# Kernel optimization log

Measured on AMD Instinct MI355X. Metric: run time of the kernel, lower is better.

Reference implementation:

```python
import jax, jax.numpy as jnp
import numpy as np

N = 500_000
B = 8192
D = 128
EPS = 1e-5


def setup_inputs() -> dict:
    key = jax.random.key(0)
    ks = jax.random.split(key, 8)
    h = jax.random.normal(ks[0], (N, D), dtype=jnp.float32)
    batch = jnp.sort(jax.random.randint(ks[1], (N,), 0, B)).astype(jnp.int64)
    vn_h = jax.random.normal(ks[2], (B, D), dtype=jnp.float32)
    # layer 0 MLP params: Linear(D,D) -> LayerNorm(D) -> ReLU -> Linear(D,D)
    W1 = jax.random.normal(ks[3], (D, D), dtype=jnp.float32) * 0.02
    b1 = jnp.zeros((D,), dtype=jnp.float32)
    ln_g = jnp.ones((D,), dtype=jnp.float32)
    ln_b = jnp.zeros((D,), dtype=jnp.float32)
    W2 = jax.random.normal(ks[4], (D, D), dtype=jnp.float32) * 0.02
    b2 = jnp.zeros((D,), dtype=jnp.float32)
    return {"h": h, "batch": batch, "vn_h": vn_h, "W1": W1, "b1": b1,
            "ln_g": ln_g, "ln_b": ln_b, "W2": W2, "b2": b2}


def _layernorm(x, g, b):
    mu = jnp.mean(x, axis=-1, keepdims=True)
    var = jnp.mean(jnp.square(x - mu), axis=-1, keepdims=True)
    return (x - mu) * jax.lax.rsqrt(var + EPS) * g + b


def reference(h, batch, vn_h, W1, b1, ln_g, ln_b, W2, b2):
    batch = batch.astype(jnp.int32)
    # global_mean_pool: segment mean of node features per graph  [B, D]
    seg_sum = jax.ops.segment_sum(h, batch, num_segments=B)
    counts = jax.ops.segment_sum(jnp.ones((h.shape[0],), h.dtype), batch, num_segments=B)
    pooled = seg_sum / jnp.maximum(counts, 1.0)[:, None]
    vn_h_new = pooled + vn_h
    # vn MLP: Linear -> LayerNorm -> ReLU -> Linear
    x = vn_h_new @ W1.T + b1
    x = jax.nn.relu(_layernorm(x, ln_g, ln_b))
    vn_out = x @ W2.T + b2                      # [B, D]
    h_out = h + vn_out[batch]                   # broadcast gather back to nodes
    return h_out, vn_out
```

## Files before the change

### kernel.cpp

```cpp
#include <hip/hip_runtime.h>

#define DIM 128
#define EPS 1e-5f

typedef short           bf16x8 __attribute__((ext_vector_type(8)));
typedef unsigned short  u16x8  __attribute__((ext_vector_type(8)));
typedef float           f32x4  __attribute__((ext_vector_type(4)));

__device__ __forceinline__ unsigned short f2b(float f) {
    unsigned int u = __builtin_bit_cast(unsigned int, f);
    unsigned int r = (u + 0x7FFFu + ((u >> 16) & 1u)) >> 16;
    return (unsigned short)r;
}
__device__ __forceinline__ bf16x8 ldw8(const float* __restrict__ p) {
    f32x4 a = *reinterpret_cast<const f32x4*>(p);
    f32x4 b = *reinterpret_cast<const f32x4*>(p + 4);
    bf16x8 r;
    #pragma unroll
    for (int j = 0; j < 4; ++j) {
        r[j]     = (short)f2b(a[j]);
        r[j + 4] = (short)f2b(b[j]);
    }
    return r;
}

__global__ __launch_bounds__(256) void k_fused(
    const float* __restrict__ h, const int* __restrict__ batch,
    const float* __restrict__ vn,
    const float* __restrict__ W1, const float* __restrict__ b1,
    const float* __restrict__ lng, const float* __restrict__ lnb,
    const float* __restrict__ W2, const float* __restrict__ b2v,
    float* __restrict__ vn_out, float* __restrict__ h_out, int n_nodes)
{
    __shared__ int sb[17];
    __shared__ unsigned short xtile[16][136];
    __shared__ float vtile[16][132];

    const int tid = threadIdx.x;
    const int G0  = blockIdx.x * 16;

    if (tid < 17) {
        const int target = G0 + tid;
        int lo = 0, hi = n_nodes;
        while (lo < hi) {
            int mid = (lo + hi) >> 1;
            if (batch[mid] < target) lo = mid + 1; else hi = mid;
        }
        sb[tid] = lo;
    }
    __syncthreads();

    const int gi = tid >> 4;
    const int j  = tid & 15;
    const int s = sb[gi], e = sb[gi + 1];

    f32x4 a0 = (f32x4){0.f, 0.f, 0.f, 0.f};
    f32x4 a1 = (f32x4){0.f, 0.f, 0.f, 0.f};
    for (int n = s; n < e; ++n) {
        const float* p = h + (size_t)n * DIM + j * 8;
        a0 += *reinterpret_cast<const f32x4*>(p);
        a1 += *reinterpret_cast<const f32x4*>(p + 4);
    }
    const int cnt = e - s;
    const float inv = 1.0f / (float)(cnt > 1 ? cnt : 1);
    const float* vp = vn + (size_t)(G0 + gi) * DIM + j * 8;
    f32x4 v0 = *reinterpret_cast<const f32x4*>(vp);
    f32x4 v1 = *reinterpret_cast<const f32x4*>(vp + 4);
    u16x8 xv;
    #pragma unroll
    for (int q = 0; q < 4; ++q) {
        xv[q]     = f2b(fmaf(a0[q], inv, v0[q]));
        xv[q + 4] = f2b(fmaf(a1[q], inv, v1[q]));
    }
    *reinterpret_cast<u16x8*>(&xtile[gi][j * 8]) = xv;
    __syncthreads();

    if (tid < 64) {
        const int lane  = tid;
        const int row16 = lane & 15;
        const int kgrp  = lane >> 4;

        bf16x8 afrag[4];
        #pragma unroll
        for (int kk = 0; kk < 4; ++kk)
            afrag[kk] = *reinterpret_cast<const bf16x8*>(&xtile[row16][kgrp * 8 + kk * 32]);

        f32x4 acc[8];
        #pragma unroll
        for (int t = 0; t < 8; ++t) acc[t] = (f32x4){0.f, 0.f, 0.f, 0.f};
        #pragma unroll
        for (int t = 0; t < 8; ++t) {
            const float* wp = W1 + (size_t)(t * 16 + row16) * DIM + kgrp * 8;
            #pragma unroll
            for (int kk = 0; kk < 4; ++kk) {
                bf16x8 bfrag = ldw8(wp + kk * 32);
                acc[t] = __builtin_amdgcn_mfma_f32_16x16x32_bf16(afrag[kk], bfrag, acc[t], 0, 0, 0);
            }
        }

        float b1f[8], gf[8], bf_[8], b2f8[8];
        #pragma unroll
        for (int t = 0; t < 8; ++t) {
            const int f = t * 16 + row16;
            b1f[t]  = b1[f];
            gf[t]   = lng[f];
            bf_[t]  = lnb[f];
            b2f8[t] = b2v[f];
        }
        #pragma unroll
        for (int t = 0; t < 8; ++t)
            #pragma unroll
            for (int r = 0; r < 4; ++r) acc[t][r] += b1f[t];

        #pragma unroll
        for (int r = 0; r < 4; ++r) {
            float sm = 0.f, ss = 0.f;
            #pragma unroll
            for (int t = 0; t < 8; ++t) { sm += acc[t][r]; ss += acc[t][r] * acc[t][r]; }
            #pragma unroll
            for (int m = 1; m <= 8; m <<= 1) {
                sm += __shfl_xor(sm, m);
                ss += __shfl_xor(ss, m);
            }
            const float mu  = sm * (1.0f / 128.0f);
            const float var = ss * (1.0f / 128.0f) - mu * mu;
            const float rs  = rsqrtf(var + EPS);
            const int   gm  = kgrp * 4 + r;
            #pragma unroll
            for (int t = 0; t < 8; ++t) {
                float z = (acc[t][r] - mu) * rs * gf[t] + bf_[t];
                z = fmaxf(z, 0.f);
                xtile[gm][t * 16 + row16] = f2b(z);
            }
        }

        bf16x8 afrag2[4];
        #pragma unroll
        for (int kk = 0; kk < 4; ++kk)
            afrag2[kk] = *reinterpret_cast<const bf16x8*>(&xtile[row16][kgrp * 8 + kk * 32]);

        f32x4 acc2[8];
        #pragma unroll
        for (int t = 0; t < 8; ++t) acc2[t] = (f32x4){0.f, 0.f, 0.f, 0.f};
        #pragma unroll
        for (int t = 0; t < 8; ++t) {
            const float* wp = W2 + (size_t)(t * 16 + row16) * DIM + kgrp * 8;
            #pragma unroll
            for (int kk = 0; kk < 4; ++kk) {
                bf16x8 bfrag = ldw8(wp + kk * 32);
                acc2[t] = __builtin_amdgcn_mfma_f32_16x16x32_bf16(afrag2[kk], bfrag, acc2[t], 0, 0, 0);
            }
        }

        #pragma unroll
        for (int r = 0; r < 4; ++r) {
            const int gm = kgrp * 4 + r;
            #pragma unroll
            for (int t = 0; t < 8; ++t)
                vtile[gm][t * 16 + row16] = acc2[t][r] + b2f8[t];
        }
    }
    __syncthreads();

    {
        const float* src = &vtile[gi][j * 8];
        float* dst = vn_out + (size_t)(G0 + gi) * DIM + j * 8;
        *reinterpret_cast<f32x4*>(dst)     = *reinterpret_cast<const f32x4*>(src);
        *reinterpret_cast<f32x4*>(dst + 4) = *reinterpret_cast<const f32x4*>(src + 4);
    }

    f32x4 w0 = *reinterpret_cast<const f32x4*>(&vtile[gi][j * 8]);
    f32x4 w1 = *reinterpret_cast<const f32x4*>(&vtile[gi][j * 8 + 4]);
    for (int n = s; n < e; ++n) {
        const float* p = h + (size_t)n * DIM + j * 8;
        f32x4 h0 = *reinterpret_cast<const f32x4*>(p);
        f32x4 h1 = *reinterpret_cast<const f32x4*>(p + 4);
        float* op = h_out + (size_t)n * DIM + j * 8;
        __builtin_nontemporal_store(h0 + w0, reinterpret_cast<f32x4*>(op));
        __builtin_nontemporal_store(h1 + w1, reinterpret_cast<f32x4*>(op + 4));
    }
}

extern "C" void kernel_launch(void* const* d_in, const int* in_sizes, int n_in,
                              void* d_out, int out_size, void* d_ws, size_t ws_size,
                              hipStream_t stream)
{
    const float* h    = (const float*)d_in[0];
    const int*   bat  = (const int*)d_in[1];
    const float* vn   = (const float*)d_in[2];
    const float* W1   = (const float*)d_in[3];
    const float* b1   = (const float*)d_in[4];
    const float* lng  = (const float*)d_in[5];
    const float* lnb  = (const float*)d_in[6];
    const float* W2   = (const float*)d_in[7];
    const float* b2v  = (const float*)d_in[8];

    const int n_nodes = in_sizes[0] / DIM;
    const int nb      = in_sizes[2] / DIM;

    float* out    = (float*)d_out;
    float* h_out  = out;
    float* vn_out = out + (size_t)n_nodes * DIM;

    k_fused<<<nb / 16, 256, 0, stream>>>(h, bat, vn, W1, b1, lng, lnb,
                                         W2, b2v, vn_out, h_out, n_nodes);
}
```

Measured before the change: 149.7 us.

## Precompute segment bounds and halve graphs per block with split-row streaming

Adds a separate kernel that computes segment boundaries from the sorted batch array in one pass, replacing the per-block binary searches. The fused kernel now handles 8 graphs per block instead of 16. Each graph gets 32 threads that split its node rows into two interleaved halves, each unrolled two rows deep, and the partial sums are combined with a lane shuffle. The MFMA tile rows 8-15 are zero-filled. The aim is more memory-level parallelism and twice as many blocks for the bandwidth-bound pooling and broadcast passes. The cost is an extra launch, half of every MFMA tile doing wasted work, and twice as many blocks each re-reading the weights.

```diff
diff --git a/kernel.cpp b/kernel.cpp
--- a/kernel.cpp
+++ b/kernel.cpp
@@ -2,8 +2,10 @@
 
 #define DIM 128
 #define EPS 1e-5f
+#define GPB 8
 
 typedef short           bf16x8 __attribute__((ext_vector_type(8)));
+typedef unsigned short  u16x4  __attribute__((ext_vector_type(4)));
 typedef unsigned short  u16x8  __attribute__((ext_vector_type(8)));
 typedef float           f32x4  __attribute__((ext_vector_type(4)));
 
@@ -24,61 +26,89 @@
     return r;
 }
 
+__global__ __launch_bounds__(256) void k_bounds(
+    const int* __restrict__ batch, int* __restrict__ bounds, int n_nodes, int nb)
+{
+    const int idx = blockIdx.x * blockDim.x + threadIdx.x;
+    if (idx > n_nodes) return;
+    const int cur  = (idx < n_nodes) ? batch[idx] : nb;
+    const int prev = (idx > 0) ? batch[idx - 1] : -1;
+    for (int b = prev + 1; b <= cur; ++b) bounds[b] = idx;
+}
+
 __global__ __launch_bounds__(256) void k_fused(
-    const float* __restrict__ h, const int* __restrict__ batch,
+    const float* __restrict__ h, const int* __restrict__ bounds,
     const float* __restrict__ vn,
     const float* __restrict__ W1, const float* __restrict__ b1,
     const float* __restrict__ lng, const float* __restrict__ lnb,
     const float* __restrict__ W2, const float* __restrict__ b2v,
     float* __restrict__ vn_out, float* __restrict__ h_out, int n_nodes)
 {
-    __shared__ int sb[17];
+    __shared__ int sb[GPB + 1];
     __shared__ unsigned short xtile[16][136];
     __shared__ float vtile[16][132];
 
     const int tid = threadIdx.x;
-    const int G0  = blockIdx.x * 16;
-
-    if (tid < 17) {
-        const int target = G0 + tid;
-        int lo = 0, hi = n_nodes;
-        while (lo < hi) {
-            int mid = (lo + hi) >> 1;
-            if (batch[mid] < target) lo = mid + 1; else hi = mid;
-        }
-        sb[tid] = lo;
+    const int G0  = blockIdx.x * GPB;
+
+    if (tid < GPB + 1) sb[tid] = bounds[G0 + tid];
+
+    {
+        const int zr = 8 + (tid >> 5);
+        const int zc = (tid & 31) * 4;
+        *reinterpret_cast<u16x4*>(&xtile[zr][zc]) = (u16x4){0, 0, 0, 0};
     }
     __syncthreads();
 
-    const int gi = tid >> 4;
-    const int j  = tid & 15;
+    const int gi   = tid >> 5;
+    const int l32  = tid & 31;
+    const int rsub = l32 >> 4;
+    const int j    = l32 & 15;
     const int s = sb[gi], e = sb[gi + 1];
 
-    f32x4 a0 = (f32x4){0.f, 0.f, 0.f, 0.f};
-    f32x4 a1 = (f32x4){0.f, 0.f, 0.f, 0.f};
-    for (int n = s; n < e; ++n) {
-        const float* p = h + (size_t)n * DIM + j * 8;
-        a0 += *reinterpret_cast<const f32x4*>(p);
-        a1 += *reinterpret_cast<const f32x4*>(p + 4);
-    }
-    const int cnt = e - s;
-    const float inv = 1.0f / (float)(cnt > 1 ? cnt : 1);
-    const float* vp = vn + (size_t)(G0 + gi) * DIM + j * 8;
-    f32x4 v0 = *reinterpret_cast<const f32x4*>(vp);
-    f32x4 v1 = *reinterpret_cast<const f32x4*>(vp + 4);
-    u16x8 xv;
+    const f32x4 z4 = (f32x4){0.f, 0.f, 0.f, 0.f};
+    f32x4 p0 = z4, p1 = z4, q0 = z4, q1 = z4;
+    int n = s + rsub;
+    for (; n + 2 < e; n += 4) {
+        const float* r0 = h + (size_t)n * DIM + j * 8;
+        const float* r1 = r0 + 2 * DIM;
+        f32x4 x0 = *reinterpret_cast<const f32x4*>(r0);
+        f32x4 x1 = *reinterpret_cast<const f32x4*>(r0 + 4);
+        f32x4 y0 = *reinterpret_cast<const f32x4*>(r1);
+        f32x4 y1 = *reinterpret_cast<const f32x4*>(r1 + 4);
+        p0 += x0; p1 += x1; q0 += y0; q1 += y1;
+    }
+    if (n < e) {
+        const float* r0 = h + (size_t)n * DIM + j * 8;
+        p0 += *reinterpret_cast<const f32x4*>(r0);
+        p1 += *reinterpret_cast<const f32x4*>(r0 + 4);
+    }
+    p0 += q0; p1 += q1;
     #pragma unroll
-    for (int q = 0; q < 4; ++q) {
-        xv[q]     = f2b(fmaf(a0[q], inv, v0[q]));
-        xv[q + 4] = f2b(fmaf(a1[q], inv, v1[q]));
-    }
-    *reinterpret_cast<u16x8*>(&xtile[gi][j * 8]) = xv;
+    for (int c = 0; c < 4; ++c) {
+        p0[c] += __shfl_xor(p0[c], 16);
+        p1[c] += __shfl_xor(p1[c], 16);
+    }
+
+    if (rsub == 0) {
+        const int cnt = e - s;
+        const float inv = 1.0f / (float)(cnt > 1 ? cnt : 1);
+        const float* vp = vn + (size_t)(G0 + gi) * DIM + j * 8;
+        f32x4 v0 = *reinterpret_cast<const f32x4*>(vp);
+        f32x4 v1 = *reinterpret_cast<const f32x4*>(vp + 4);
+        u16x8 xv;
+        #pragma unroll
+        for (int q = 0; q < 4; ++q) {
+            xv[q]     = f2b(fmaf(p0[q], inv, v0[q]));
+            xv[q + 4] = f2b(fmaf(p1[q], inv, v1[q]));
+        }
+        *reinterpret_cast<u16x8*>(&xtile[gi][j * 8]) = xv;
+    }
     __syncthreads();
 
     if (tid < 64) {
-        const int lane  = tid;
-        const int row16 = lane & 15;
-        const int kgrp  = lane >> 4;
+        const int row16 = tid & 15;
+        const int kgrp  = tid >> 4;
 
         bf16x8 afrag[4];
         #pragma unroll
@@ -163,21 +193,35 @@
     __syncthreads();
 
     {
-        const float* src = &vtile[gi][j * 8];
-        float* dst = vn_out + (size_t)(G0 + gi) * DIM + j * 8;
-        *reinterpret_cast<f32x4*>(dst)     = *reinterpret_cast<const f32x4*>(src);
-        *reinterpret_cast<f32x4*>(dst + 4) = *reinterpret_cast<const f32x4*>(src + 4);
+        float* dst = vn_out + (size_t)(G0 + gi) * DIM + l32 * 4;
+        *reinterpret_cast<f32x4*>(dst) =
+            *reinterpret_cast<const f32x4*>(&vtile[gi][l32 * 4]);
     }
 
     f32x4 w0 = *reinterpret_cast<const f32x4*>(&vtile[gi][j * 8]);
     f32x4 w1 = *reinterpret_cast<const f32x4*>(&vtile[gi][j * 8 + 4]);
-    for (int n = s; n < e; ++n) {
-        const float* p = h + (size_t)n * DIM + j * 8;
-        f32x4 h0 = *reinterpret_cast<const f32x4*>(p);
-        f32x4 h1 = *reinterpret_cast<const f32x4*>(p + 4);
-        float* op = h_out + (size_t)n * DIM + j * 8;
-        __builtin_nontemporal_store(h0 + w0, reinterpret_cast<f32x4*>(op));
-        __builtin_nontemporal_store(h1 + w1, reinterpret_cast<f32x4*>(op + 4));
+    n = s + rsub;
+    for (; n + 2 < e; n += 4) {
+        const float* r0 = h + (size_t)n * DIM + j * 8;
+        const float* r1 = r0 + 2 * DIM;
+        f32x4 x0 = *reinterpret_cast<const f32x4*>(r0);
+        f32x4 x1 = *reinterpret_cast<const f32x4*>(r0 + 4);
+        f32x4 y0 = *reinterpret_cast<const f32x4*>(r1);
+        f32x4 y1 = *reinterpret_cast<const f32x4*>(r1 + 4);
+        float* o0 = h_out + (size_t)n * DIM + j * 8;
+        float* o1 = o0 + 2 * DIM;
+        __builtin_nontemporal_store(x0 + w0, reinterpret_cast<f32x4*>(o0));
+        __builtin_nontemporal_store(x1 + w1, reinterpret_cast<f32x4*>(o0 + 4));
+        __builtin_nontemporal_store(y0 + w0, reinterpret_cast<f32x4*>(o1));
+        __builtin_nontemporal_store(y1 + w1, reinterpret_cast<f32x4*>(o1 + 4));
+    }
+    if (n < e) {
+        const float* r0 = h + (size_t)n * DIM + j * 8;
+        f32x4 x0 = *reinterpret_cast<const f32x4*>(r0);
+        f32x4 x1 = *reinterpret_cast<const f32x4*>(r0 + 4);
+        float* o0 = h_out + (size_t)n * DIM + j * 8;
+        __builtin_nontemporal_store(x0 + w0, reinterpret_cast<f32x4*>(o0));
+        __builtin_nontemporal_store(x1 + w1, reinterpret_cast<f32x4*>(o0 + 4));
     }
 }
 
@@ -201,7 +245,9 @@
     float* out    = (float*)d_out;
     float* h_out  = out;
     float* vn_out = out + (size_t)n_nodes * DIM;
-
-    k_fused<<<nb / 16, 256, 0, stream>>>(h, bat, vn, W1, b1, lng, lnb,
-                                         W2, b2v, vn_out, h_out, n_nodes);
-}
+    int*   bounds = (int*)d_ws;
+
+    k_bounds<<<(n_nodes + 256) / 256, 256, 0, stream>>>(bat, bounds, n_nodes, nb);
+    k_fused<<<nb / GPB, 256, 0, stream>>>(h, bounds, vn, W1, b1, lng, lnb,
+                                          W2, b2v, vn_out, h_out, n_nodes);
+}
```

Result: slower. 162.9 us (+8.9%).
